# Kernel optimization log

Hardware: AMD Instinct MI355X
Metric: run time of the kernel (lower is better)

Reference implementation:

```python
import jax, jax.numpy as jnp
import numpy as np

D_MODEL = 1024
HEAD_DIM = 256
MEMORY_SIZE = 64
SPARSITY_RATIO = 0.1
NEG_INF = -1.0e9


def setup_inputs() -> dict:
    key = jax.random.key(0)
    ks = jax.random.split(key, 16)
    s = lambda fan_in: 1.0 / np.sqrt(fan_in)
    inp = {
        "x": jax.random.normal(ks[0], (2, 4096, D_MODEL), dtype=jnp.float32),
        # local attention head (qkv fused, no bias); weights stored [in, out]
        "local_qkv_w": jax.random.uniform(ks[1], (D_MODEL, 3 * HEAD_DIM), minval=-s(D_MODEL), maxval=s(D_MODEL)),
        # sparse global head
        "sparse_qkv_w": jax.random.uniform(ks[2], (D_MODEL, 3 * HEAD_DIM), minval=-s(D_MODEL), maxval=s(D_MODEL)),
        # memory head
        "memory_bank": jax.random.normal(ks[3], (MEMORY_SIZE, HEAD_DIM), dtype=jnp.float32),
        "memory_proj_w": jax.random.uniform(ks[4], (D_MODEL, HEAD_DIM), minval=-s(D_MODEL), maxval=s(D_MODEL)),
        "mem_out_w": jax.random.uniform(ks[5], (2 * HEAD_DIM, HEAD_DIM), minval=-s(2 * HEAD_DIM), maxval=s(2 * HEAD_DIM)),
        "mem_out_b": jax.random.uniform(ks[6], (HEAD_DIM,), minval=-s(2 * HEAD_DIM), maxval=s(2 * HEAD_DIM)),
        # prediction head
        "pred_in_w": jax.random.uniform(ks[7], (D_MODEL, HEAD_DIM), minval=-s(D_MODEL), maxval=s(D_MODEL)),
        "pred_in_b": jax.random.uniform(ks[8], (HEAD_DIM,), minval=-s(D_MODEL), maxval=s(D_MODEL)),
        "pred1_w": jax.random.uniform(ks[9], (HEAD_DIM, 2 * HEAD_DIM), minval=-s(HEAD_DIM), maxval=s(HEAD_DIM)),
        "pred1_b": jax.random.uniform(ks[10], (2 * HEAD_DIM,), minval=-s(HEAD_DIM), maxval=s(HEAD_DIM)),
        "pred2_w": jax.random.uniform(ks[11], (2 * HEAD_DIM, HEAD_DIM), minval=-s(2 * HEAD_DIM), maxval=s(2 * HEAD_DIM)),
        "pred2_b": jax.random.uniform(ks[12], (HEAD_DIM,), minval=-s(2 * HEAD_DIM), maxval=s(2 * HEAD_DIM)),
        # warboss output projection
        "warboss_w": jax.random.uniform(ks[13], (4 * HEAD_DIM, D_MODEL), minval=-s(4 * HEAD_DIM), maxval=s(4 * HEAD_DIM)),
        "warboss_b": jax.random.uniform(ks[14], (D_MODEL,), minval=-s(4 * HEAD_DIM), maxval=s(4 * HEAD_DIM)),
    }
    return inp


def _full_attention(x, qkv_w, scale):
    # x: [B,S,D] -> q,k,v: [B,S,H]
    qkv = x @ qkv_w
    q, k, v = jnp.split(qkv, 3, axis=-1)
    scores = jnp.einsum("bsh,bth->bst", q, k) * scale  # [B,S,S]
    probs = jax.nn.softmax(scores, axis=-1)
    return probs @ v


def _sparse_global_attention(x, qkv_w, scale):
    qkv = x @ qkv_w
    q, k, v = jnp.split(qkv, 3, axis=-1)
    scores = jnp.einsum("bsh,bth->bst", q, k) * scale  # [B,S,S]
    seq_len = x.shape[1]
    k_sparse = max(1, int(seq_len * SPARSITY_RATIO))
    topk_vals, _ = jax.lax.top_k(scores, k_sparse)
    kth = topk_vals[..., -1:]  # [B,S,1] threshold
    masked = jnp.where(scores >= kth, scores, NEG_INF)
    probs = jax.nn.softmax(masked, axis=-1)
    return probs @ v


def _memory_head(x, memory_bank, memory_proj_w, mem_out_w, mem_out_b):
    x_proj = x @ memory_proj_w  # [B,S,H]
    mem_scores = jnp.einsum("bsh,mh->bsm", x_proj, memory_bank)
    mem_weights = jax.nn.softmax(mem_scores, axis=-1)
    retrieved = jnp.einsum("bsm,mh->bsh", mem_weights, memory_bank)
    combined = jnp.concatenate([x_proj, retrieved], axis=-1)
    return combined @ mem_out_w + mem_out_b


def _prediction_head(x, pred_in_w, pred_in_b, pred1_w, pred1_b, pred2_w, pred2_b):
    h = x @ pred_in_w + pred_in_b
    h = h @ pred1_w + pred1_b
    h = jax.nn.gelu(h, approximate=False)
    return h @ pred2_w + pred2_b


def reference(x, local_qkv_w, sparse_qkv_w, memory_bank, memory_proj_w, mem_out_w, mem_out_b, pred_in_w, pred_in_b, pred1_w, pred1_b, pred2_w, pred2_b, warboss_w, warboss_b):
    scale = HEAD_DIM ** -0.5
    local_out = _full_attention(x, local_qkv_w, scale)
    sparse_out = _sparse_global_attention(x, sparse_qkv_w, scale)
    mem_out = _memory_head(x, memory_bank, memory_proj_w, mem_out_w, mem_out_b)
    pred_out = _prediction_head(x, pred_in_w, pred_in_b, pred1_w, pred1_b, pred2_w, pred2_b)
    combined = jnp.concatenate([local_out, sparse_out, mem_out, pred_out], axis=-1)
    return combined @ warboss_w + warboss_b
```

## Files before the change

kernel.cpp:

```cpp
#include <hip/hip_runtime.h>
#include <hip/hip_bf16.h>

typedef __attribute__((ext_vector_type(8))) _Float16 half8;
typedef __attribute__((ext_vector_type(4))) _Float16 half4v;
typedef __attribute__((ext_vector_type(4))) float f32x4;

__device__ __forceinline__ float wred_max(float v){
  #pragma unroll
  for (int o = 32; o; o >>= 1) v = fmaxf(v, __shfl_xor(v, o));
  return v;
}
__device__ __forceinline__ float wred_sum(float v){
  #pragma unroll
  for (int o = 32; o; o >>= 1) v += __shfl_xor(v, o);
  return v;
}
__device__ __forceinline__ unsigned short h2u(_Float16 h){
  unsigned short u;
  __builtin_memcpy(&u, &h, 2);
  return u;
}

#define GLOAD16(GP, LP) __builtin_amdgcn_global_load_lds( \
    (const __attribute__((address_space(1))) void*)(GP),  \
    (__attribute__((address_space(3))) void*)(LP), 16, 0, 0)

template<int BM, int BN, int OUT_F16, int ACT>
__global__ __launch_bounds__(256) void gemm_ht(
    const _Float16* __restrict__ A, long saz, int lda,
    const _Float16* __restrict__ B, long sbz, int ldb,
    void* __restrict__ Cv, long scz, int ldc,
    int K, float alpha, const float* __restrict__ bias)
{
  constexpr int FM = BM / 32, FN = BN / 32;
  __shared__ __align__(16) _Float16 Asl[BM * 32];
  __shared__ __align__(16) _Float16 Bsl[BN * 32];
  const int t = threadIdx.x;
  const int wid = t >> 6, lane = t & 63;
  const int wr = wid >> 1, wc = wid & 1;
  const int lr = lane & 15, kg = lane >> 4;
  A += (long)blockIdx.z * saz;
  B += (long)blockIdx.z * sbz;
  const long row0 = (long)blockIdx.y * BM;
  const long col0 = (long)blockIdx.x * BN;

  f32x4 acc[FM][FN];
  #pragma unroll
  for (int i = 0; i < FM; i++)
    #pragma unroll
    for (int j = 0; j < FN; j++)
      acc[i][j] = (f32x4){0.f, 0.f, 0.f, 0.f};

  const int arow_t = t >> 2, acol_t = (t & 3) * 8;

  for (int k0 = 0; k0 < K; k0 += 32){
    #pragma unroll
    for (int r = 0; r < BM / 64; r++){
      const _Float16* gp = A + (row0 + r*64 + arow_t) * (long)lda + k0 + acol_t;
      GLOAD16(gp, (char*)Asl + r*4096 + wid*1024);
    }
    #pragma unroll
    for (int r = 0; r < BN / 64; r++){
      const _Float16* gp = B + (col0 + r*64 + arow_t) * (long)ldb + k0 + acol_t;
      GLOAD16(gp, (char*)Bsl + r*4096 + wid*1024);
    }
    __syncthreads();
    half8 af[FM], bfv[FN];
    #pragma unroll
    for (int i = 0; i < FM; i++)
      af[i] = *(const half8*)((const char*)Asl + (wr*(BM/2) + i*16 + lr)*64 + kg*16);
    #pragma unroll
    for (int j = 0; j < FN; j++)
      bfv[j] = *(const half8*)((const char*)Bsl + (wc*(BN/2) + j*16 + lr)*64 + kg*16);
    #pragma unroll
    for (int i = 0; i < FM; i++)
      #pragma unroll
      for (int j = 0; j < FN; j++)
        acc[i][j] = __builtin_amdgcn_mfma_f32_16x16x32_f16(af[i], bfv[j], acc[i][j], 0, 0, 0);
    __syncthreads();
  }

  _Float16* Ch = (_Float16*)Cv + (long)blockIdx.z * scz;
  float*    Cf = (float*)Cv    + (long)blockIdx.z * scz;
  #pragma unroll
  for (int i = 0; i < FM; i++){
    #pragma unroll
    for (int j = 0; j < FN; j++){
      #pragma unroll
      for (int q = 0; q < 4; q++){
        long rr = row0 + wr*(BM/2) + i*16 + kg*4 + q;
        long cc = col0 + wc*(BN/2) + j*16 + lr;
        float val = acc[i][j][q] * alpha;
        if (bias) val += bias[cc];
        if constexpr (ACT) val = 0.5f * val * (1.0f + erff(val * 0.70710678118654752f));
        if constexpr (OUT_F16) Ch[rr*(long)ldc + cc] = (_Float16)val;
        else                   Cf[rr*(long)ldc + cc] = val;
      }
    }
  }
}

template<int BM, int BN>
__global__ __launch_bounds__(256) void gemm_pv(
    const _Float16* __restrict__ A, long saz, int lda,
    const _Float16* __restrict__ B, long sbz, int ldb,
    float* __restrict__ P, int nsplit, int Ksplit)
{
  constexpr int FM = BM / 32, FN = BN / 32;
  __shared__ __align__(16) _Float16 Asl[BM * 32];
  __shared__ __align__(16) _Float16 Bsl[BN * 32];
  const int t = threadIdx.x;
  const int wid = t >> 6, lane = t & 63;
  const int wr = wid >> 1, wc = wid & 1;
  const int lr = lane & 15, kg = lane >> 4;
  const int z = blockIdx.z, batch = z / nsplit, split = z % nsplit;
  A += (long)batch * saz;
  B += (long)batch * sbz;
  float* Pz = P + (size_t)z * (4096 * 256);
  const long row0 = (long)blockIdx.y * BM;
  const int Kbase = split * Ksplit;

  f32x4 acc[FM][FN];
  #pragma unroll
  for (int i = 0; i < FM; i++)
    #pragma unroll
    for (int j = 0; j < FN; j++)
      acc[i][j] = (f32x4){0.f, 0.f, 0.f, 0.f};

  const int arow_t = t >> 2, acol_t = (t & 3) * 8;

  for (int k0 = 0; k0 < Ksplit; k0 += 32){
    #pragma unroll
    for (int r = 0; r < BM / 64; r++){
      const _Float16* gp = A + (row0 + r*64 + arow_t) * (long)lda + Kbase + k0 + acol_t;
      GLOAD16(gp, (char*)Asl + r*4096 + wid*1024);
    }
    #pragma unroll
    for (int r = 0; r < BN / 64; r++){
      const _Float16* gp = B + (r*64 + arow_t) * (long)ldb + Kbase + k0 + acol_t;
      GLOAD16(gp, (char*)Bsl + r*4096 + wid*1024);
    }
    __syncthreads();
    half8 af[FM], bfv[FN];
    #pragma unroll
    for (int i = 0; i < FM; i++)
      af[i] = *(const half8*)((const char*)Asl + (wr*(BM/2) + i*16 + lr)*64 + kg*16);
    #pragma unroll
    for (int j = 0; j < FN; j++)
      bfv[j] = *(const half8*)((const char*)Bsl + (wc*(BN/2) + j*16 + lr)*64 + kg*16);
    #pragma unroll
    for (int i = 0; i < FM; i++)
      #pragma unroll
      for (int j = 0; j < FN; j++)
        acc[i][j] = __builtin_amdgcn_mfma_f32_16x16x32_f16(af[i], bfv[j], acc[i][j], 0, 0, 0);
    __syncthreads();
  }

  #pragma unroll
  for (int i = 0; i < FM; i++)
    #pragma unroll
    for (int j = 0; j < FN; j++)
      #pragma unroll
      for (int q = 0; q < 4; q++){
        long rr = row0 + wr*(BM/2) + i*16 + kg*4 + q;
        long cc = wc*(BN/2) + j*16 + lr;
        Pz[rr*256 + cc] = acc[i][j][q];
      }
}

__global__ __launch_bounds__(256) void reduce4(const float* __restrict__ P,
                                               _Float16* __restrict__ dst, int coff, int nq){
  int i = blockIdx.x * 256 + threadIdx.x;
  if (i >= nq) return;
  int b = i >> 18;
  int r = i & 262143;
  int row = r >> 6, col4 = r & 63;
  const float4* P4 = (const float4*)P;
  float4 s = P4[(size_t)(b*4 + 0) * 262144 + r];
  #pragma unroll
  for (int sp = 1; sp < 4; sp++){
    float4 q = P4[(size_t)(b*4 + sp) * 262144 + r];
    s.x += q.x; s.y += q.y; s.z += q.z; s.w += q.w;
  }
  half4v o;
  o[0] = (_Float16)s.x; o[1] = (_Float16)s.y; o[2] = (_Float16)s.z; o[3] = (_Float16)s.w;
  *(half4v*)(dst + ((size_t)b*4096 + row)*1024 + coff + col4*4) = o;
}

__global__ __launch_bounds__(256) void cast_xh(const float* __restrict__ in,
                                               _Float16* __restrict__ out, int n8){
  int i = blockIdx.x * 256 + threadIdx.x;
  const int stride = gridDim.x * 256;
  for (; i < n8; i += stride){
    float4 a = ((const float4*)in)[2*i];
    float4 b = ((const float4*)in)[2*i + 1];
    half8 o;
    o[0]=(_Float16)a.x; o[1]=(_Float16)a.y; o[2]=(_Float16)a.z; o[3]=(_Float16)a.w;
    o[4]=(_Float16)b.x; o[5]=(_Float16)b.y; o[6]=(_Float16)b.z; o[7]=(_Float16)b.w;
    *(half8*)(out + (size_t)i*8) = o;
  }
}

__global__ __launch_bounds__(256) void transpose_cast_w(const float* __restrict__ in, int R, int C,
                                                        _Float16* __restrict__ out){
  __shared__ float tile[32][33];
  const int c0 = blockIdx.x * 32, r0 = blockIdx.y * 32;
  const int tx = threadIdx.x & 31, ty = threadIdx.x >> 5;
  #pragma unroll
  for (int i = 0; i < 32; i += 8)
    tile[ty+i][tx] = in[(size_t)(r0+ty+i)*C + c0+tx];
  __syncthreads();
  #pragma unroll
  for (int i = 0; i < 32; i += 8)
    out[(size_t)(c0+ty+i)*R + r0+tx] = (_Float16)tile[tx][ty+i];
}

__global__ __launch_bounds__(256) void transpose_h(
    const _Float16* __restrict__ in, long in_z, int ld_in,
    _Float16* __restrict__ out, long out_z, int ld_out)
{
  __shared__ _Float16 tile[32][34];
  const _Float16* ip = in + (long)blockIdx.z * in_z;
  _Float16* op = out + (long)blockIdx.z * out_z;
  const int c0 = blockIdx.x * 32, r0 = blockIdx.y * 32;
  const int tx = threadIdx.x & 31, ty = threadIdx.x >> 5;
  #pragma unroll
  for (int i = 0; i < 32; i += 8)
    tile[ty+i][tx] = ip[(long)(r0+ty+i)*ld_in + c0+tx];
  __syncthreads();
  #pragma unroll
  for (int i = 0; i < 32; i += 8)
    op[(long)(c0+ty+i)*ld_out + r0+tx] = tile[tx][ty+i];
}

__global__ __launch_bounds__(256) void softmax_f16row(_Float16* __restrict__ sc){
  __shared__ float red[4], red2[4];
  const int t = threadIdx.x, lane = t & 63, wid = t >> 6;
  _Float16* p = sc + (size_t)blockIdx.x * 4096;
  half8 a = ((const half8*)p)[t*2];
  half8 b = ((const half8*)p)[t*2 + 1];
  float v[16];
  #pragma unroll
  for (int e = 0; e < 8; e++){ v[e] = (float)a[e]; v[8+e] = (float)b[e]; }
  float m = v[0];
  #pragma unroll
  for (int e = 1; e < 16; e++) m = fmaxf(m, v[e]);
  m = wred_max(m);
  if (lane == 0) red[wid] = m;
  __syncthreads();
  m = fmaxf(fmaxf(red[0], red[1]), fmaxf(red[2], red[3]));
  float s = 0.f;
  #pragma unroll
  for (int e = 0; e < 16; e++){ v[e] = expf(v[e] - m); s += v[e]; }
  s = wred_sum(s);
  if (lane == 0) red2[wid] = s;
  __syncthreads();
  s = red2[0] + red2[1] + red2[2] + red2[3];
  const float inv = 1.0f / s;
  half8 oa, ob;
  #pragma unroll
  for (int e = 0; e < 8; e++){ oa[e] = (_Float16)(v[e]*inv); ob[e] = (_Float16)(v[8+e]*inv); }
  ((half8*)p)[t*2]     = oa;
  ((half8*)p)[t*2 + 1] = ob;
}

__global__ __launch_bounds__(256) void sparse_softmax16(_Float16* __restrict__ sc, int ksel){
  __shared__ unsigned hist4[4][256];
  __shared__ unsigned hrev[256];
  __shared__ unsigned suf[257];
  __shared__ unsigned wtot[4];
  __shared__ int selb;
  __shared__ float red[4], red2[4];
  const int t = threadIdx.x, lane = t & 63, wid = t >> 6;
  _Float16* p = sc + (size_t)blockIdx.x * 4096;
  half8 a = ((const half8*)p)[t*2];
  half8 b = ((const half8*)p)[t*2 + 1];
  float v[16]; unsigned kk[16];
  #pragma unroll
  for (int e = 0; e < 8; e++){
    unsigned short u0 = h2u(a[e]);
    unsigned short u1 = h2u(b[e]);
    kk[e]   = (u0 & 0x8000u) ? (unsigned)(unsigned short)~u0 : (unsigned)(u0 | 0x8000u);
    kk[8+e] = (u1 & 0x8000u) ? (unsigned)(unsigned short)~u1 : (unsigned)(u1 | 0x8000u);
    v[e] = (float)a[e]; v[8+e] = (float)b[e];
  }
  float m = v[0];
  #pragma unroll
  for (int e = 1; e < 16; e++) m = fmaxf(m, v[e]);
  m = wred_max(m);
  if (lane == 0) red[wid] = m;
  __syncthreads();
  m = fmaxf(fmaxf(red[0], red[1]), fmaxf(red[2], red[3]));

  ((uint4*)hist4)[t] = (uint4){0u,0u,0u,0u};
  __syncthreads();
  #pragma unroll
  for (int e = 0; e < 16; e++) atomicAdd(&hist4[wid][kk[e] >> 8], 1u);
  __syncthreads();
  {
    unsigned h = hist4[0][t] + hist4[1][t] + hist4[2][t] + hist4[3][t];
    hrev[t] = h;
  }
  __syncthreads();
  unsigned x = hrev[255 - t];
  #pragma unroll
  for (int o = 1; o < 64; o <<= 1){
    unsigned y = __shfl_up(x, o);
    if (lane >= o) x += y;
  }
  if (lane == 63) wtot[wid] = x;
  __syncthreads();
  #pragma unroll
  for (int w = 0; w < 4; w++) if (w < wid) x += wtot[w];
  suf[255 - t] = x;
  if (t == 0) suf[256] = 0u;
  __syncthreads();
  const unsigned ku = (unsigned)ksel;
  if (suf[t] >= ku && suf[t+1] < ku) selb = t;
  __syncthreads();
  const int b1 = selb;
  const unsigned rem = ku - suf[b1+1];
  __syncthreads();

  ((uint4*)hist4)[t] = (uint4){0u,0u,0u,0u};
  __syncthreads();
  #pragma unroll
  for (int e = 0; e < 16; e++)
    if ((int)(kk[e] >> 8) == b1) atomicAdd(&hist4[wid][kk[e] & 255u], 1u);
  __syncthreads();
  {
    unsigned h = hist4[0][t] + hist4[1][t] + hist4[2][t] + hist4[3][t];
    hrev[t] = h;
  }
  __syncthreads();
  x = hrev[255 - t];
  #pragma unroll
  for (int o = 1; o < 64; o <<= 1){
    unsigned y = __shfl_up(x, o);
    if (lane >= o) x += y;
  }
  if (lane == 63) wtot[wid] = x;
  __syncthreads();
  #pragma unroll
  for (int w = 0; w < 4; w++) if (w < wid) x += wtot[w];
  suf[255 - t] = x;
  if (t == 0) suf[256] = 0u;
  __syncthreads();
  if (suf[t] >= rem && suf[t+1] < rem) selb = t;
  __syncthreads();
  const unsigned Tkey = ((unsigned)b1 << 8) | (unsigned)selb;

  float ev[16];
  float s = 0.f;
  #pragma unroll
  for (int e = 0; e < 16; e++){
    ev[e] = (kk[e] >= Tkey) ? expf(v[e] - m) : 0.f;
    s += ev[e];
  }
  s = wred_sum(s);
  if (lane == 0) red2[wid] = s;
  __syncthreads();
  s = red2[0] + red2[1] + red2[2] + red2[3];
  const float inv = 1.0f / s;
  half8 o0, o1;
  #pragma unroll
  for (int e = 0; e < 8; e++){
    o0[e] = (_Float16)(ev[e]   * inv);
    o1[e] = (_Float16)(ev[8+e] * inv);
  }
  ((half8*)p)[t*2]     = o0;
  ((half8*)p)[t*2 + 1] = o1;
}

__global__ __launch_bounds__(256) void msoftmax64(const float* __restrict__ mscore,
                                                  _Float16* __restrict__ mprob){
  const int t = threadIdx.x, lane = t & 63, wid = t >> 6;
  const size_t row = (size_t)blockIdx.x * 4 + wid;
  float v = mscore[row*64 + lane];
  float m = wred_max(v);
  float e = expf(v - m);
  float s = wred_sum(e);
  mprob[row*64 + lane] = (_Float16)(e / s);
}

extern "C" void kernel_launch(void* const* d_in, const int* in_sizes, int n_in,
                              void* d_out, int out_size, void* d_ws, size_t ws_size,
                              hipStream_t stream)
{
  const float* x             = (const float*)d_in[0];
  const float* local_qkv_w   = (const float*)d_in[1];
  const float* sparse_qkv_w  = (const float*)d_in[2];
  const float* memory_bank   = (const float*)d_in[3];
  const float* memory_proj_w = (const float*)d_in[4];
  const float* mem_out_w     = (const float*)d_in[5];
  const float* mem_out_b     = (const float*)d_in[6];
  const float* pred_in_w     = (const float*)d_in[7];
  const float* pred_in_b     = (const float*)d_in[8];
  const float* pred1_w       = (const float*)d_in[9];
  const float* pred1_b       = (const float*)d_in[10];
  const float* pred2_w       = (const float*)d_in[11];
  const float* pred2_b       = (const float*)d_in[12];
  const float* warboss_w     = (const float*)d_in[13];
  const float* warboss_b     = (const float*)d_in[14];
  float* out = (float*)d_out;

  char* wsb = (char*)d_ws;
  _Float16*  scores_h = (_Float16*)wsb;
  _Float16*  x_h      = (_Float16*)wsb;
  _Float16*  mem_cat  = (_Float16*)(wsb + 16777216);
  _Float16*  h_in     = (_Float16*)(wsb + 25165824);
  _Float16*  h1       = (_Float16*)(wsb + 29360128);
  float*     mscore   = (float*)(wsb + 37748736);
  _Float16*  mprob    = (_Float16*)(wsb + 39845888);
  _Float16*  qkv_l    = (_Float16*)(wsb + 67108864);
  _Float16*  qkv_s    = (_Float16*)(wsb + 79691776);
  _Float16*  Vt       = (_Float16*)(wsb + 92274688);
  _Float16*  comb     = (_Float16*)(wsb + 96468992);
  _Float16*  lqkvT    = (_Float16*)(wsb + 113246208);
  _Float16*  sqkvT    = lqkvT  + 786432;
  _Float16*  mprojT   = sqkvT  + 786432;
  _Float16*  moutT    = mprojT + 262144;
  _Float16*  pinT     = moutT  + 131072;
  _Float16*  p1T      = pinT   + 262144;
  _Float16*  p2T      = p1T    + 131072;
  _Float16*  wbT      = p2T    + 131072;
  _Float16*  bank_h   = wbT    + 1048576;
  _Float16*  bankT_h  = bank_h + 16384;

  const dim3 blk(256);
  const float scale = 0.0625f;
  const long QZ  = (long)4096 * 768;
  const long VZ  = (long)256 * 4096;
  const long SZH = (long)4096 * 4096;

  cast_xh<<<dim3(2048), blk, 0, stream>>>(x, x_h, 1048576);
  cast_xh<<<dim3(8), blk, 0, stream>>>(memory_bank, bank_h, 2048);
  transpose_cast_w<<<dim3(24,32), blk, 0, stream>>>(local_qkv_w,  1024,  768, lqkvT);
  transpose_cast_w<<<dim3(24,32), blk, 0, stream>>>(sparse_qkv_w, 1024,  768, sqkvT);
  transpose_cast_w<<<dim3( 8,32), blk, 0, stream>>>(memory_proj_w,1024,  256, mprojT);
  transpose_cast_w<<<dim3( 8,16), blk, 0, stream>>>(mem_out_w,     512,  256, moutT);
  transpose_cast_w<<<dim3( 8,32), blk, 0, stream>>>(pred_in_w,    1024,  256, pinT);
  transpose_cast_w<<<dim3(16, 8), blk, 0, stream>>>(pred1_w,       256,  512, p1T);
  transpose_cast_w<<<dim3( 8,16), blk, 0, stream>>>(pred2_w,       512,  256, p2T);
  transpose_cast_w<<<dim3(32,32), blk, 0, stream>>>(warboss_w,    1024, 1024, wbT);
  transpose_cast_w<<<dim3( 8, 2), blk, 0, stream>>>(memory_bank,    64,  256, bankT_h);

  gemm_ht<128,128,1,0><<<dim3(6,64,2), blk, 0, stream>>>(x_h,0,1024, lqkvT,786432,1024,
                                                         qkv_l,6291456,768, 1024, 1.f, nullptr);

  gemm_ht<64,64,1,0><<<dim3(4,128), blk, 0, stream>>>(x_h,0,1024, mprojT,0,1024, mem_cat,0,512, 1024, 1.f, nullptr);
  gemm_ht<64,64,0,0><<<dim3(1,128), blk, 0, stream>>>(mem_cat,0,512, bank_h,0,256, (void*)mscore,0,64, 256, 1.f, nullptr);
  msoftmax64<<<dim3(2048), blk, 0, stream>>>(mscore, mprob);
  gemm_ht<64,64,1,0><<<dim3(4,128), blk, 0, stream>>>(mprob,0,64, bankT_h,0,64, mem_cat+256,0,512, 64, 1.f, nullptr);
  gemm_ht<64,64,1,0><<<dim3(4,128), blk, 0, stream>>>(mem_cat,0,512, moutT,0,512, comb+512,0,1024, 512, 1.f, mem_out_b);

  gemm_ht<64,64,1,0><<<dim3(4,128), blk, 0, stream>>>(x_h,0,1024, pinT,0,1024, h_in,0,256, 1024, 1.f, pred_in_b);
  gemm_ht<64,128,1,1><<<dim3(4,128), blk, 0, stream>>>(h_in,0,256, p1T,0,256, h1,0,512, 256, 1.f, pred1_b);
  gemm_ht<64,64,1,0><<<dim3(4,128), blk, 0, stream>>>(h1,0,512, p2T,0,512, comb+768,0,1024, 512, 1.f, pred2_b);

  transpose_h<<<dim3(8,128,2), blk, 0, stream>>>(qkv_l+512, QZ, 768, Vt, VZ, 4096);
  gemm_ht<128,128,1,0><<<dim3(32,32,2), blk, 0, stream>>>(qkv_l,QZ,768, qkv_l+256,QZ,768,
                                                          (void*)scores_h,SZH,4096, 256, scale, nullptr);
  softmax_f16row<<<dim3(8192), blk, 0, stream>>>(scores_h);
  gemm_pv<64,256><<<dim3(1,64,8), blk, 0, stream>>>(scores_h,SZH,4096, Vt,VZ,4096, out, 4, 1024);
  reduce4<<<dim3(2048), blk, 0, stream>>>(out, comb, 0, 524288);

  transpose_h<<<dim3(8,128,2), blk, 0, stream>>>(qkv_s+512, QZ, 768, Vt, VZ, 4096);
  gemm_ht<128,128,1,0><<<dim3(32,32,2), blk, 0, stream>>>(qkv_s,QZ,768, qkv_s+256,QZ,768,
                                                          (void*)scores_h,SZH,4096, 256, scale, nullptr);
  sparse_softmax16<<<dim3(8192), blk, 0, stream>>>(scores_h, 409);
  gemm_pv<64,256><<<dim3(1,64,8), blk, 0, stream>>>(scores_h,SZH,4096, Vt,VZ,4096, out, 4, 1024);
  reduce4<<<dim3(2048), blk, 0, stream>>>(out, comb, 256, 524288);

  gemm_ht<128,128,0,0><<<dim3(8,64), blk, 0, stream>>>(comb,0,1024, wbT,0,1024, (void*)out,0,1024, 1024, 1.f, warboss_b);
}
```

Measured before the change: 425.6 us.

## Fuse softmax exponentiation into PV GEMM and defer normalization to split-K reduce

Softmax kernels now only compute per-row max, sum and (for sparse) the top-k threshold, writing a small stats buffer instead of rewriting the 4096x4096 score matrix. The PV GEMM loads raw scores, applies exp(v-m) with the threshold mask while staging into LDS, and the split-K reduce divides by the row sum. Split-K partials are stored as fp16 rather than fp32, halving reduction traffic. This removes a full read-modify-write of the score matrix per head, at the cost of synchronous A-tile loads in the GEMM and some fp16 precision risk in partials.

```diff
diff --git a/kernel.cpp b/kernel.cpp
--- a/kernel.cpp
+++ b/kernel.cpp
@@ -19,6 +19,11 @@
   unsigned short u;
   __builtin_memcpy(&u, &h, 2);
   return u;
+}
+__device__ __forceinline__ float u2hf(unsigned short u){
+  _Float16 h;
+  __builtin_memcpy(&h, &u, 2);
+  return (float)h;
 }
 
 #define GLOAD16(GP, LP) __builtin_amdgcn_global_load_lds( \
@@ -100,11 +105,12 @@
   }
 }
 
-template<int BM, int BN>
-__global__ __launch_bounds__(256) void gemm_pv(
+template<int BM, int BN, int SPARSE>
+__global__ __launch_bounds__(256) void gemm_pv_exp(
     const _Float16* __restrict__ A, long saz, int lda,
     const _Float16* __restrict__ B, long sbz, int ldb,
-    float* __restrict__ P, int nsplit, int Ksplit)
+    const float4* __restrict__ mlthr,
+    _Float16* __restrict__ Ph, int nsplit, int Ksplit)
 {
   constexpr int FM = BM / 32, FN = BN / 32;
   __shared__ __align__(16) _Float16 Asl[BM * 32];
@@ -116,10 +122,15 @@
   const int z = blockIdx.z, batch = z / nsplit, split = z % nsplit;
   A += (long)batch * saz;
   B += (long)batch * sbz;
-  float* Pz = P + (size_t)z * (4096 * 256);
+  _Float16* Pz = Ph + (size_t)z * (4096 * 256);
   const long row0 = (long)blockIdx.y * BM;
   const int Kbase = split * Ksplit;
 
+  const long arow = row0 + (t >> 2);
+  const float4 mt = mlthr[(long)batch*4096 + arow];
+  const float m = mt.x, thr = mt.z;
+  const _Float16* Ap = A + arow * (long)lda + Kbase + (t & 3) * 8;
+
   f32x4 acc[FM][FN];
   #pragma unroll
   for (int i = 0; i < FM; i++)
@@ -130,15 +141,23 @@
   const int arow_t = t >> 2, acol_t = (t & 3) * 8;
 
   for (int k0 = 0; k0 < Ksplit; k0 += 32){
-    #pragma unroll
-    for (int r = 0; r < BM / 64; r++){
-      const _Float16* gp = A + (row0 + r*64 + arow_t) * (long)lda + Kbase + k0 + acol_t;
-      GLOAD16(gp, (char*)Asl + r*4096 + wid*1024);
-    }
     #pragma unroll
     for (int r = 0; r < BN / 64; r++){
       const _Float16* gp = B + (r*64 + arow_t) * (long)ldb + Kbase + k0 + acol_t;
       GLOAD16(gp, (char*)Bsl + r*4096 + wid*1024);
+    }
+    {
+      half8 ld = *(const half8*)(Ap + k0);
+      half8 st;
+      #pragma unroll
+      for (int e = 0; e < 8; e++){
+        float v = (float)ld[e];
+        float ev;
+        if constexpr (SPARSE) ev = (v >= thr) ? __expf(v - m) : 0.f;
+        else                  ev = __expf(v - m);
+        st[e] = (_Float16)ev;
+      }
+      *(half8*)((char*)Asl + t*16) = st;
     }
     __syncthreads();
     half8 af[FM], bfv[FN];
@@ -164,26 +183,28 @@
       for (int q = 0; q < 4; q++){
         long rr = row0 + wr*(BM/2) + i*16 + kg*4 + q;
         long cc = wc*(BN/2) + j*16 + lr;
-        Pz[rr*256 + cc] = acc[i][j][q];
+        Pz[rr*256 + cc] = (_Float16)acc[i][j][q];
       }
 }
 
-__global__ __launch_bounds__(256) void reduce4(const float* __restrict__ P,
-                                               _Float16* __restrict__ dst, int coff, int nq){
+__global__ __launch_bounds__(256) void reduce4h(const _Float16* __restrict__ Ph,
+                                                const float4* __restrict__ mlthr,
+                                                _Float16* __restrict__ dst, int coff, int nq){
   int i = blockIdx.x * 256 + threadIdx.x;
   if (i >= nq) return;
   int b = i >> 18;
   int r = i & 262143;
   int row = r >> 6, col4 = r & 63;
-  const float4* P4 = (const float4*)P;
-  float4 s = P4[(size_t)(b*4 + 0) * 262144 + r];
-  #pragma unroll
-  for (int sp = 1; sp < 4; sp++){
-    float4 q = P4[(size_t)(b*4 + sp) * 262144 + r];
-    s.x += q.x; s.y += q.y; s.z += q.z; s.w += q.w;
-  }
+  float sx = 0.f, sy = 0.f, sz = 0.f, sw = 0.f;
+  #pragma unroll
+  for (int sp = 0; sp < 4; sp++){
+    half4v p = *(const half4v*)(Ph + (((size_t)(b*4 + sp)*4096 + row)*256 + col4*4));
+    sx += (float)p[0]; sy += (float)p[1]; sz += (float)p[2]; sw += (float)p[3];
+  }
+  const float inv = 1.0f / mlthr[(long)b*4096 + row].y;
   half4v o;
-  o[0] = (_Float16)s.x; o[1] = (_Float16)s.y; o[2] = (_Float16)s.z; o[3] = (_Float16)s.w;
+  o[0] = (_Float16)(sx*inv); o[1] = (_Float16)(sy*inv);
+  o[2] = (_Float16)(sz*inv); o[3] = (_Float16)(sw*inv);
   *(half4v*)(dst + ((size_t)b*4096 + row)*1024 + coff + col4*4) = o;
 }
 
@@ -233,10 +254,11 @@
     op[(long)(c0+ty+i)*ld_out + r0+tx] = tile[tx][ty+i];
 }
 
-__global__ __launch_bounds__(256) void softmax_f16row(_Float16* __restrict__ sc){
+__global__ __launch_bounds__(256) void rowstat_local(const _Float16* __restrict__ sc,
+                                                     float4* __restrict__ mlthr){
   __shared__ float red[4], red2[4];
   const int t = threadIdx.x, lane = t & 63, wid = t >> 6;
-  _Float16* p = sc + (size_t)blockIdx.x * 4096;
+  const _Float16* p = sc + (size_t)blockIdx.x * 4096;
   half8 a = ((const half8*)p)[t*2];
   half8 b = ((const half8*)p)[t*2 + 1];
   float v[16];
@@ -251,20 +273,18 @@
   m = fmaxf(fmaxf(red[0], red[1]), fmaxf(red[2], red[3]));
   float s = 0.f;
   #pragma unroll
-  for (int e = 0; e < 16; e++){ v[e] = expf(v[e] - m); s += v[e]; }
+  for (int e = 0; e < 16; e++) s += __expf(v[e] - m);
   s = wred_sum(s);
   if (lane == 0) red2[wid] = s;
   __syncthreads();
-  s = red2[0] + red2[1] + red2[2] + red2[3];
-  const float inv = 1.0f / s;
-  half8 oa, ob;
-  #pragma unroll
-  for (int e = 0; e < 8; e++){ oa[e] = (_Float16)(v[e]*inv); ob[e] = (_Float16)(v[8+e]*inv); }
-  ((half8*)p)[t*2]     = oa;
-  ((half8*)p)[t*2 + 1] = ob;
-}
-
-__global__ __launch_bounds__(256) void sparse_softmax16(_Float16* __restrict__ sc, int ksel){
+  if (t == 0){
+    s = red2[0] + red2[1] + red2[2] + red2[3];
+    mlthr[blockIdx.x] = make_float4(m, s, -3.0e38f, 0.f);
+  }
+}
+
+__global__ __launch_bounds__(256) void rowstat_sparse(const _Float16* __restrict__ sc,
+                                                      float4* __restrict__ mlthr, int ksel){
   __shared__ unsigned hist4[4][256];
   __shared__ unsigned hrev[256];
   __shared__ unsigned suf[257];
@@ -272,7 +292,7 @@
   __shared__ int selb;
   __shared__ float red[4], red2[4];
   const int t = threadIdx.x, lane = t & 63, wid = t >> 6;
-  _Float16* p = sc + (size_t)blockIdx.x * 4096;
+  const _Float16* p = sc + (size_t)blockIdx.x * 4096;
   half8 a = ((const half8*)p)[t*2];
   half8 b = ((const half8*)p)[t*2 + 1];
   float v[16]; unsigned kk[16];
@@ -297,10 +317,7 @@
   #pragma unroll
   for (int e = 0; e < 16; e++) atomicAdd(&hist4[wid][kk[e] >> 8], 1u);
   __syncthreads();
-  {
-    unsigned h = hist4[0][t] + hist4[1][t] + hist4[2][t] + hist4[3][t];
-    hrev[t] = h;
-  }
+  hrev[t] = hist4[0][t] + hist4[1][t] + hist4[2][t] + hist4[3][t];
   __syncthreads();
   unsigned x = hrev[255 - t];
   #pragma unroll
@@ -328,10 +345,7 @@
   for (int e = 0; e < 16; e++)
     if ((int)(kk[e] >> 8) == b1) atomicAdd(&hist4[wid][kk[e] & 255u], 1u);
   __syncthreads();
-  {
-    unsigned h = hist4[0][t] + hist4[1][t] + hist4[2][t] + hist4[3][t];
-    hrev[t] = h;
-  }
+  hrev[t] = hist4[0][t] + hist4[1][t] + hist4[2][t] + hist4[3][t];
   __syncthreads();
   x = hrev[255 - t];
   #pragma unroll
@@ -349,27 +363,21 @@
   if (suf[t] >= rem && suf[t+1] < rem) selb = t;
   __syncthreads();
   const unsigned Tkey = ((unsigned)b1 << 8) | (unsigned)selb;
-
-  float ev[16];
+  const unsigned short tu = (Tkey & 0x8000u) ? (unsigned short)(Tkey & 0x7fffu)
+                                             : (unsigned short)~Tkey;
+  const float thr = u2hf(tu);
+
   float s = 0.f;
   #pragma unroll
-  for (int e = 0; e < 16; e++){
-    ev[e] = (kk[e] >= Tkey) ? expf(v[e] - m) : 0.f;
-    s += ev[e];
-  }
+  for (int e = 0; e < 16; e++)
+    s += (v[e] >= thr) ? __expf(v[e] - m) : 0.f;
   s = wred_sum(s);
   if (lane == 0) red2[wid] = s;
   __syncthreads();
-  s = red2[0] + red2[1] + red2[2] + red2[3];
-  const float inv = 1.0f / s;
-  half8 o0, o1;
-  #pragma unroll
-  for (int e = 0; e < 8; e++){
-    o0[e] = (_Float16)(ev[e]   * inv);
-    o1[e] = (_Float16)(ev[8+e] * inv);
-  }
-  ((half8*)p)[t*2]     = o0;
-  ((half8*)p)[t*2 + 1] = o1;
+  if (t == 0){
+    s = red2[0] + red2[1] + red2[2] + red2[3];
+    mlthr[blockIdx.x] = make_float4(m, s, thr, 0.f);
+  }
 }
 
 __global__ __launch_bounds__(256) void msoftmax64(const float* __restrict__ mscore,
@@ -403,6 +411,7 @@
   const float* warboss_w     = (const float*)d_in[13];
   const float* warboss_b     = (const float*)d_in[14];
   float* out = (float*)d_out;
+  _Float16* Ph = (_Float16*)d_out;
 
   char* wsb = (char*)d_ws;
   _Float16*  scores_h = (_Float16*)wsb;
@@ -426,6 +435,7 @@
   _Float16*  wbT      = p2T    + 131072;
   _Float16*  bank_h   = wbT    + 1048576;
   _Float16*  bankT_h  = bank_h + 16384;
+  float4*    mlthr    = (float4*)(bankT_h + 16384);
 
   const dim3 blk(256);
   const float scale = 0.0625f;
@@ -461,16 +471,16 @@
   transpose_h<<<dim3(8,128,2), blk, 0, stream>>>(qkv_l+512, QZ, 768, Vt, VZ, 4096);
   gemm_ht<128,128,1,0><<<dim3(32,32,2), blk, 0, stream>>>(qkv_l,QZ,768, qkv_l+256,QZ,768,
                                                           (void*)scores_h,SZH,4096, 256, scale, nullptr);
-  softmax_f16row<<<dim3(8192), blk, 0, stream>>>(scores_h);
-  gemm_pv<64,256><<<dim3(1,64,8), blk, 0, stream>>>(scores_h,SZH,4096, Vt,VZ,4096, out, 4, 1024);
-  reduce4<<<dim3(2048), blk, 0, stream>>>(out, comb, 0, 524288);
+  rowstat_local<<<dim3(8192), blk, 0, stream>>>(scores_h, mlthr);
+  gemm_pv_exp<64,256,0><<<dim3(1,64,8), blk, 0, stream>>>(scores_h,SZH,4096, Vt,VZ,4096, mlthr, Ph, 4, 1024);
+  reduce4h<<<dim3(2048), blk, 0, stream>>>(Ph, mlthr, comb, 0, 524288);
 
   transpose_h<<<dim3(8,128,2), blk, 0, stream>>>(qkv_s+512, QZ, 768, Vt, VZ, 4096);
   gemm_ht<128,128,1,0><<<dim3(32,32,2), blk, 0, stream>>>(qkv_s,QZ,768, qkv_s+256,QZ,768,
                                                           (void*)scores_h,SZH,4096, 256, scale, nullptr);
-  sparse_softmax16<<<dim3(8192), blk, 0, stream>>>(scores_h, 409);
-  gemm_pv<64,256><<<dim3(1,64,8), blk, 0, stream>>>(scores_h,SZH,4096, Vt,VZ,4096, out, 4, 1024);
-  reduce4<<<dim3(2048), blk, 0, stream>>>(out, comb, 256, 524288);
+  rowstat_sparse<<<dim3(8192), blk, 0, stream>>>(scores_h, mlthr, 409);
+  gemm_pv_exp<64,256,1><<<dim3(1,64,8), blk, 0, stream>>>(scores_h,SZH,4096, Vt,VZ,4096, mlthr, Ph, 4, 1024);
+  reduce4h<<<dim3(2048), blk, 0, stream>>>(Ph, mlthr, comb, 256, 524288);
 
   gemm_ht<128,128,0,0><<<dim3(8,64), blk, 0, stream>>>(comb,0,1024, wbT,0,1024, (void*)out,0,1024, 1024, 1.f, warboss_b);
 }
```

Measured after the change: 403.1 us. -5.3%, faster.
